# Kernel tuning notes

Measured on AMD Instinct MI355X. Metric: run time of the kernel, lower is better.

The kernel has to match this reference:

```python
import jax, jax.numpy as jnp
import numpy as np
from jax.scipy.special import xlogy

B, S, DIM, H = 2, 2048, 1024, 16
D = DIM // H          # head_dim = 64
B1 = B2 = 8           # monarch block sizes (hard-coded in source)
F = S // (B1 * B2)    # frames
NUM_ITERS = 2
EPS = 1e-6


def setup_inputs() -> dict:
    key = jax.random.key(0)
    ks = jax.random.split(key, 4)
    x = jax.random.normal(ks[0], (B, S, DIM), jnp.float32)
    # interleaved-pair RoPE tables, shape (S, D)
    pos = jnp.arange(S, dtype=jnp.float32)
    inv = 1.0 / (10000.0 ** (jnp.arange(0, D, 2, dtype=jnp.float32) / D))
    ang = pos[:, None] * inv[None, :]
    cos = jnp.repeat(jnp.cos(ang), 2, axis=-1)
    sin = jnp.repeat(jnp.sin(ang), 2, axis=-1)
    sc = 0.02
    wq = jax.random.normal(ks[1], (DIM, DIM), jnp.float32) * sc
    wk = jax.random.normal(ks[2], (DIM, DIM), jnp.float32) * sc
    wv = jax.random.normal(ks[3], (DIM, DIM), jnp.float32) * sc
    gq = jnp.ones((D,), jnp.float32)
    gk = jnp.ones((D,), jnp.float32)
    return {"x": x, "cos": cos, "sin": sin, "wq": wq, "wk": wk, "wv": wv,
            "gq": gq, "gk": gk}


def _rmsnorm(x, g, eps=EPS):
    return x * jax.lax.rsqrt(jnp.mean(x * x, axis=-1, keepdims=True) + eps) * g


def _rope(x, cos, sin):
    # x: (B,S,H,D); cos/sin: (S,D); rotate interleaved pairs
    xp = x.reshape(*x.shape[:-1], D // 2, 2)
    xr = jnp.stack([-xp[..., 1], xp[..., 0]], axis=-1).reshape(x.shape)
    return x * cos[None, :, None, :] + xr * sin[None, :, None, :]


def _monarch_forward(x, cos, sin, wq, wk, wv, gq, gk):
    b, s, dim = x.shape
    scale = D ** (-0.25)  # sm_scale_sqrt
    q = _rmsnorm((x @ wq.T).reshape(b, s, H, D), gq)
    k = _rmsnorm((x @ wk.T).reshape(b, s, H, D), gk)
    q = _rope(q, cos, sin) * scale
    k = _rope(k, cos, sin) * scale
    v = (x @ wv.T).reshape(b, s, H, D)

    # (b, frame, i=b1, j=b2, h, d)
    q = q.reshape(b, F, B1, B2, H, D)
    k = k.reshape(b, F, B1, B2, H, D)
    v = v.reshape(b, F, B1, B2, H, D)

    # causal frame mask: query frame g attends kv frames f <= g
    fmask = jnp.arange(F)[None, :] <= jnp.arange(F)[:, None]          # (G,F)
    mb = fmask[None, None, :, :, None, None, None]                    # (1,1,G,F,1,1,1)
    eye = jnp.eye(B1, dtype=x.dtype)                                   # (k,i)
    # L: (b,h,g,f,j,k,i), initialized to identity on allowed frames
    L = jnp.broadcast_to(jnp.where(mb, eye, 0.0), (b, H, F, F, B2, B1, B1))
    NEG = jnp.finfo(x.dtype).min

    R = None
    for _ in range(NUM_ITERS):
        aR = jnp.einsum('bhgfjki,bgijhd->bgfkjhd', L, q)
        bR = jnp.einsum('bgfkjhd,bfklhd->bhgfkjl', aR, k)
        cR = jnp.einsum('bhgfjki->bhgfkj', L)[..., None]
        R = jax.nn.softmax(bR / (cR + EPS), axis=-1)                  # (b,h,g,f,k,j,l)
        aL = jnp.einsum('bhgfkjl,bfklhd->bgfjkhd', R, k)
        bL = jnp.einsum('bgfjkhd,bgijhd->bhgfjki', aL, q)
        # cL[b,h,g,f,j,k] = sum_l xlogy(R)[b,h,g,f,k,j,l]
        cL = jnp.swapaxes(jnp.sum(xlogy(R, R), axis=-1), -1, -2)[..., None]
        M = jnp.where(mb, bL - cL, NEG)                               # (b,h,g,f,j,k,i)
        Mt = jnp.transpose(M, (0, 1, 2, 4, 6, 3, 5))                  # (b,h,g,j,i,f,k)
        Lf = jax.nn.softmax(Mt.reshape(b, H, F, B2, B1, F * B1), axis=-1)
        L = jnp.transpose(Lf.reshape(b, H, F, B2, B1, F, B1), (0, 1, 2, 5, 3, 6, 4))

    o = jnp.einsum('bhgfkjl,bfklhd->bgfjkhd', R, v)
    out = jnp.einsum('bhgfjki,bgfjkhd->bgijhd', L, o)                 # (b,G,i,j,h,d)
    return out.reshape(b, s, dim)


def reference(x, cos, sin, wq, wk, wv, gq, gk):
    return _monarch_forward(x, cos, sin, wq, wk, wv, gq, gk)
```

## Files before the change

### kernel.cpp

```cpp
#include <hip/hip_runtime.h>
#include <stdint.h>

typedef _Float16 f16;
typedef _Float16 half8 __attribute__((ext_vector_type(8)));
typedef _Float16 half4v __attribute__((ext_vector_type(4)));
typedef float f32x4 __attribute__((ext_vector_type(4)));

#define DEV static __device__ __forceinline__

DEV f32x4 mfma16(half8 a, half8 b, f32x4 c) {
  return __builtin_amdgcn_mfma_f32_16x16x32_f16(a, b, c, 0, 0, 0);
}

DEV void cp16(const f16* g, f16* l) {
  __builtin_amdgcn_global_load_lds(
      (const __attribute__((address_space(1))) void*)g,
      (__attribute__((address_space(3))) void*)l, 16, 0, 0);
}


__global__ __launch_bounds__(256) void k_cast(
    const float* __restrict__ x, const float* __restrict__ wq,
    const float* __restrict__ wk, const float* __restrict__ wv,
    f16* __restrict__ xh, f16* __restrict__ wcat) {
  const int64_t nx4 = 4194304 / 4;
  const int64_t nw4 = 1048576 / 4;
  int64_t stride = (int64_t)gridDim.x * blockDim.x;
  for (int64_t i = (int64_t)blockIdx.x * blockDim.x + threadIdx.x;
       i < nx4 + 3 * nw4; i += stride) {
    const float* src; f16* dst; int64_t off;
    if (i < nx4) { src = x; dst = xh; off = i; }
    else {
      int64_t r = i - nx4;
      int ws_ = (int)(r / nw4);
      off = r - (int64_t)ws_ * nw4;
      src = (ws_ == 0) ? wq : ((ws_ == 1) ? wk : wv);
      dst = wcat + (int64_t)ws_ * 1048576;
    }
    float4 v = ((const float4*)src)[off];
    half4v hh; hh[0] = (f16)v.x; hh[1] = (f16)v.y; hh[2] = (f16)v.z; hh[3] = (f16)v.w;
    ((half4v*)dst)[off] = hh;
  }
}

__global__ __launch_bounds__(256) void k_gemm(
    const f16* __restrict__ A, const f16* __restrict__ Bm,
    float* __restrict__ P) {
  __shared__ f16 As[128 * 64];
  __shared__ f16 Bs[128 * 64];
  const int t = threadIdx.x;
  const int wave = t >> 6, lane = t & 63, quad = lane >> 4, ln = lane & 15;
  const int tM = blockIdx.x / 24, tN = blockIdx.x % 24;
  const int wm = wave >> 1, wn = wave & 1;
  f32x4 acc[4][4];
#pragma unroll
  for (int a = 0; a < 4; ++a)
#pragma unroll
    for (int b = 0; b < 4; ++b) { f32x4 z = {0.f, 0.f, 0.f, 0.f}; acc[a][b] = z; }
  const int srow = t >> 3;
  const int c = (t & 7) ^ (srow & 7);
  const f16* Ag = A + (int64_t)(tM * 128 + srow) * 1024 + c * 8;
  const f16* Bg = Bm + (int64_t)(tN * 128 + srow) * 1024 + c * 8;
  for (int kt = 0; kt < 16; ++kt) {
    __syncthreads();
#pragma unroll
    for (int it = 0; it < 4; ++it) {
      cp16(Ag + (int64_t)it * 32 * 1024 + kt * 64, &As[it * 2048 + wave * 512]);
      cp16(Bg + (int64_t)it * 32 * 1024 + kt * 64, &Bs[it * 2048 + wave * 512]);
    }
    __syncthreads();
#pragma unroll
    for (int ks = 0; ks < 2; ++ks) {
      const int cs = ((ks * 4 + quad) ^ (ln & 7)) * 8;
      half8 bf[4];
#pragma unroll
      for (int tn = 0; tn < 4; ++tn)
        bf[tn] = *(const half8*)&Bs[(wn * 64 + tn * 16 + ln) * 64 + cs];
#pragma unroll
      for (int tm = 0; tm < 4; ++tm) {
        half8 af = *(const half8*)&As[(wm * 64 + tm * 16 + ln) * 64 + cs];
#pragma unroll
        for (int tn = 0; tn < 4; ++tn)
          acc[tm][tn] = mfma16(af, bf[tn], acc[tm][tn]);
      }
    }
  }
#pragma unroll
  for (int tm = 0; tm < 4; ++tm)
#pragma unroll
    for (int tn = 0; tn < 4; ++tn)
#pragma unroll
      for (int r2 = 0; r2 < 4; ++r2) {
        int row = tM * 128 + wm * 64 + tm * 16 + quad * 4 + r2;
        int col = tN * 128 + wn * 64 + tn * 16 + ln;
        P[(int64_t)row * 3072 + col] = acc[tm][tn][r2];
      }
}

__global__ __launch_bounds__(256) void k_epilogue(
    const float* __restrict__ P, const float* __restrict__ cosg,
    const float* __restrict__ sing, const float* __restrict__ gq,
    const float* __restrict__ gk, f16* __restrict__ qh,
    f16* __restrict__ kh, f16* __restrict__ vth) {
  __shared__ f16 vbuf[64 * 72];
  const int t = threadIdx.x;
  const int bid = blockIdx.x;
  const int st = bid & 31, h = (bid >> 5) & 15, b = bid >> 9;
  const int r = t >> 2, qt = t & 3, c0 = qt * 16;
  const int s = st * 64 + r;
  const int64_t rowbase = (int64_t)(b * 2048 + s) * 3072;
  const float scale = 0.35355339059327373f;
#pragma unroll
  for (int m = 0; m < 2; ++m) {
    const float* gv = (m == 0) ? gq : gk;
    const int colbase = m * 1024 + h * 64 + c0;
    float xv[16];
#pragma unroll
    for (int c = 0; c < 4; ++c) {
      float4 v4 = *(const float4*)&P[rowbase + colbase + c * 4];
      xv[c * 4 + 0] = v4.x; xv[c * 4 + 1] = v4.y;
      xv[c * 4 + 2] = v4.z; xv[c * 4 + 3] = v4.w;
    }
    float ss = 0.f;
#pragma unroll
    for (int c = 0; c < 16; ++c) ss += xv[c] * xv[c];
    ss += __shfl_xor(ss, 1, 64);
    ss += __shfl_xor(ss, 2, 64);
    float rs = rsqrtf(ss * (1.f / 64.f) + 1e-6f);
    alignas(16) f16 res[16];
#pragma unroll
    for (int ci = 0; ci < 16; ci += 2) {
      int d0 = c0 + ci, d1 = d0 + 1;
      float av = xv[ci] * rs * gv[d0];
      float bv = xv[ci + 1] * rs * gv[d1];
      float c0v = cosg[s * 64 + d0], c1v = cosg[s * 64 + d1];
      float s0v = sing[s * 64 + d0], s1v = sing[s * 64 + d1];
      res[ci]     = (f16)((av * c0v - bv * s0v) * scale);
      res[ci + 1] = (f16)((bv * c1v + av * s1v) * scale);
    }
    f16* dst = ((m == 0) ? qh : kh) + (int64_t)((b * 16 + h) * 2048 + s) * 64 + c0;
    *(half8*)dst = *(const half8*)&res[0];
    *(half8*)(dst + 8) = *(const half8*)&res[8];
  }
  {
    const int colbase = 2048 + h * 64 + c0;
#pragma unroll
    for (int c = 0; c < 4; ++c) {
      float4 v4 = *(const float4*)&P[rowbase + colbase + c * 4];
      vbuf[(c0 + c * 4 + 0) * 72 + r] = (f16)v4.x;
      vbuf[(c0 + c * 4 + 1) * 72 + r] = (f16)v4.y;
      vbuf[(c0 + c * 4 + 2) * 72 + r] = (f16)v4.z;
      vbuf[(c0 + c * 4 + 3) * 72 + r] = (f16)v4.w;
    }
    __syncthreads();
    const int d = t >> 2, sc = qt * 16;
    alignas(16) f16 tmp[16];
#pragma unroll
    for (int ci = 0; ci < 16; ++ci) tmp[ci] = vbuf[d * 72 + sc + ci];
    f16* dst = vth + (int64_t)(((b * 16 + h) * 32 + st) * 64 + d) * 64 + sc;
    *(half8*)dst = *(const half8*)&tmp[0];
    *(half8*)(dst + 8) = *(const half8*)&tmp[8];
  }
}

__global__ __launch_bounds__(64) void k_phase(
    const f16* __restrict__ qh, const f16* __restrict__ kh,
    float* __restrict__ Lg, f16* __restrict__ Rg,
    const f16* __restrict__ Pg, int iter) {
  __shared__ float Sw[4416];
  const int lane = threadIdx.x;
  const int quad = lane >> 4, ln = lane & 15;
  const int jr = lane >> 3, kr = lane & 7;

  const int bh = blockIdx.x / 528;
  const int rem = blockIdx.x - bh * 528;
  int g = (int)((sqrtf(8.f * (float)rem + 1.f) - 1.f) * 0.5f);
  while ((g + 1) * (g + 2) / 2 <= rem) ++g;
  while (g * (g + 1) / 2 > rem) --g;
  const int f = rem - g * (g + 1) / 2;

  const f16* qg = qh + (int64_t)(bh * 2048 + g * 64) * 64;
  const f16* kf = kh + (int64_t)(bh * 2048 + f * 64) * 64;
  const int64_t sbase = ((int64_t)bh * 528 + ((g * (g + 1)) >> 1) + f) * 512;
  float* Lp = Lg + sbase;

  half8 afr[2][4], bfr[2][4];
#pragma unroll
  for (int ks = 0; ks < 2; ++ks)
#pragma unroll
    for (int t4 = 0; t4 < 4; ++t4) {
      afr[ks][t4] = *(const half8*)&qg[(t4 * 16 + ln) * 64 + ks * 32 + quad * 8];
      bfr[ks][t4] = *(const half8*)&kf[(t4 * 16 + ln) * 64 + ks * 32 + quad * 8];
    }
  float p[8], cR = 0.f;
  if (iter) {
    half8 ph = *(const half8*)&Pg[sbase + lane * 8];
    p[0] = (float)ph[0]; p[2] = (float)ph[1]; p[4] = (float)ph[2]; p[6] = (float)ph[3];
    p[1] = (float)ph[4]; p[3] = (float)ph[5]; p[5] = (float)ph[6]; p[7] = (float)ph[7];
#pragma unroll
    for (int i = 0; i < 8; ++i) cR += p[i];
  }
  f32x4 acc[4][4];
#pragma unroll
  for (int a = 0; a < 4; ++a)
#pragma unroll
    for (int b = 0; b < 4; ++b) { f32x4 z = {0.f, 0.f, 0.f, 0.f}; acc[a][b] = z; }
#pragma unroll
  for (int ks = 0; ks < 2; ++ks)
#pragma unroll
    for (int mt = 0; mt < 4; ++mt)
#pragma unroll
      for (int nt = 0; nt < 4; ++nt)
        acc[mt][nt] = mfma16(afr[ks][mt], bfr[ks][nt], acc[mt][nt]);
  const int wbase = (quad >> 1) * 552 + (quad & 1) * 272 + (ln >> 3) * 8 + (ln & 7);
#pragma unroll
  for (int mt = 0; mt < 4; ++mt)
#pragma unroll
    for (int nt = 0; nt < 4; ++nt)
#pragma unroll
      for (int r2 = 0; r2 < 4; ++r2)
        Sw[wbase + mt * 1104 + nt * 16 + r2 * 68] = acc[mt][nt][r2];
  __syncthreads();
  float Sr[8][8];
  const int rb = jr * 68 + kr * 8;
#pragma unroll
  for (int i = 0; i < 8; ++i) {
    *(float4*)&Sr[i][0] = *(const float4*)&Sw[i * 552 + rb];
    *(float4*)&Sr[i][4] = *(const float4*)&Sw[i * 552 + rb + 4];
  }
  float va[8];
  if (!iter) {
    float4 d0 = *(const float4*)&Sw[kr * 552 + rb];
    float4 d1 = *(const float4*)&Sw[kr * 552 + rb + 4];
    va[0] = d0.x; va[1] = d0.y; va[2] = d0.z; va[3] = d0.w;
    va[4] = d1.x; va[5] = d1.y; va[6] = d1.z; va[7] = d1.w;
    const float sc = 1.f / (1.f + 1e-6f);
#pragma unroll
    for (int l = 0; l < 8; ++l) va[l] *= sc;
  } else {
    float bR[8];
#pragma unroll
    for (int l = 0; l < 8; ++l) bR[l] = 0.f;
#pragma unroll
    for (int i = 0; i < 8; ++i)
#pragma unroll
      for (int l = 0; l < 8; ++l) bR[l] += p[i] * Sr[i][l];
    const float rc = 1.f / (cR + 1e-6f);
#pragma unroll
    for (int l = 0; l < 8; ++l) va[l] = bR[l] * rc;
  }
  float mx = va[0];
#pragma unroll
  for (int l = 1; l < 8; ++l) mx = fmaxf(mx, va[l]);
  float ex[8], sm = 0.f;
#pragma unroll
  for (int l = 0; l < 8; ++l) { ex[l] = __expf(va[l] - mx); sm += ex[l]; }
  const float inv = 1.f / sm;
  float rr[8], rl = 0.f;
#pragma unroll
  for (int l = 0; l < 8; ++l) {
    rr[l] = ex[l] * inv;
    rl += rr[l] * __logf(fmaxf(rr[l], 1e-30f));
  }
  if (iter) {
    half8 r8;
#pragma unroll
    for (int l = 0; l < 8; ++l) r8[l] = (f16)rr[l];
    *(half8*)&Rg[sbase + kr * 64 + jr * 8] = r8;
  }
  float bl[8];
#pragma unroll
  for (int i = 0; i < 8; ++i) {
    float s = 0.f;
#pragma unroll
    for (int l = 0; l < 8; ++l) s += rr[l] * Sr[i][l];
    bl[i] = s - rl;
  }
  *(float4*)&Lp[lane * 8]     = *(const float4*)&bl[0];
  *(float4*)&Lp[lane * 8 + 4] = *(const float4*)&bl[4];
}

__global__ __launch_bounds__(256) void k_probs(
    const float* __restrict__ Lg, f16* __restrict__ Pg) {
  __shared__ float Ls[32 * 546];
  __shared__ float stt[128];
  const int t = threadIdx.x;
  const int g = 31 - (blockIdx.x & 31), bh = blockIdx.x >> 5;
  const int64_t sb = ((int64_t)bh * 528 + ((g * (g + 1)) >> 1)) * 512;
  const float* Lp = Lg + sb;
  for (int f = 0; f <= g; ++f) {
    const int o = 2 * t;
    *(float2*)&Ls[f * 546 + (o >> 6) * 68 + (o & 63)] = *(const float2*)&Lp[f * 512 + o];
  }
  __syncthreads();
  {
    const int p = t >> 2, sub = t & 3;
    const int base = (p >> 3) * 68 + (p & 7);
    float mx = -1e30f;
    for (int f = sub; f <= g; f += 4)
#pragma unroll
      for (int k_ = 0; k_ < 8; ++k_)
        mx = fmaxf(mx, Ls[f * 546 + base + k_ * 8]);
    mx = fmaxf(mx, __shfl_xor(mx, 1, 64));
    mx = fmaxf(mx, __shfl_xor(mx, 2, 64));
    float se = 0.f;
    for (int f = sub; f <= g; f += 4)
#pragma unroll
      for (int k_ = 0; k_ < 8; ++k_)
        se += __expf(Ls[f * 546 + base + k_ * 8] - mx);
    se += __shfl_xor(se, 1, 64);
    se += __shfl_xor(se, 2, 64);
    if (sub == 0) { stt[p * 2] = mx; stt[p * 2 + 1] = 1.f / se; }
  }
  __syncthreads();
  {
    const int r = t & 63, fq = t >> 6;
    const int j = r >> 3, k_ = r & 7;
    float mx[8], inv[8];
#pragma unroll
    for (int i = 0; i < 8; ++i) {
      mx[i] = stt[(j * 8 + i) * 2];
      inv[i] = stt[(j * 8 + i) * 2 + 1];
    }
    for (int fb = fq; fb <= g; fb += 4) {
      const float* row = &Ls[fb * 546 + j * 68 + k_ * 8];
      float pr[8];
#pragma unroll
      for (int i = 0; i < 8; ++i) pr[i] = __expf(row[i] - mx[i]) * inv[i];
      half8 st8;
      st8[0] = (f16)pr[0]; st8[1] = (f16)pr[2]; st8[2] = (f16)pr[4]; st8[3] = (f16)pr[6];
      st8[4] = (f16)pr[1]; st8[5] = (f16)pr[3]; st8[6] = (f16)pr[5]; st8[7] = (f16)pr[7];
      *(half8*)&Pg[sb + (int64_t)fb * 512 + r * 8] = st8;
    }
  }
}

__global__ __launch_bounds__(512) void k_out(
    const f16* __restrict__ Pg, const f16* __restrict__ Rg,
    const f16* __restrict__ vth, float* __restrict__ out) {
  __shared__ float red[64 * 64];
  const int t = threadIdx.x;
  const int wave = t >> 6, lane = t & 63, quad = lane >> 4, ln = lane & 15;
  const int fg = wave >> 2, dw = wave & 3;
  const int bh = blockIdx.x >> 4, G = blockIdx.x & 15;
  const int jl = ln & 7, ih = ln >> 3;
  const f16* vb = vth + ((int64_t)bh * 32 * 64 + dw * 16 + ln) * 64;

#pragma unroll 1
  for (int ph = 0; ph < 2; ++ph) {
    const int g = ph ? G : 31 - G;
    const int64_t sbase = ((int64_t)bh * 528 + ((g * (g + 1)) >> 1)) * 512;
    const f16* Pp = Pg + sbase;
    const f16* Rp = Rg + sbase;
    f32x4 oacc[4];
#pragma unroll
    for (int mt = 0; mt < 4; ++mt) { f32x4 z = {0.f, 0.f, 0.f, 0.f}; oacc[mt] = z; }

    half8 vA0, vA1, rA0, rA1; half4v pA0, pA1;
    half8 vB0, vB1, rB0, rB1; half4v pB0, pB1;
    auto loadit = [&](int f, half8& v0, half8& v1, half8& r0, half8& r1,
                      half4v& p0, half4v& p1) {
      const f16* Pf = Pp + f * 512;
      const f16* Rf = Rp + f * 512;
      const f16* vf = vb + (int64_t)f * 64 * 64;
      v0 = *(const half8*)&vf[quad * 8];
      v1 = *(const half8*)&vf[32 + quad * 8];
      r0 = *(const half8*)&Rf[quad * 64 + jl * 8];
      r1 = *(const half8*)&Rf[(4 + quad) * 64 + jl * 8];
      p0 = *(const half4v*)&Pf[jl * 64 + quad * 8 + ih * 4];
      p1 = *(const half4v*)&Pf[jl * 64 + (4 + quad) * 8 + ih * 4];
    };
    auto compit = [&](half8& v0, half8& v1, half8& r0, half8& r1,
                      half4v& p0, half4v& p1) {
#pragma unroll
      for (int mt = 0; mt < 4; ++mt) {
        const f16 Lh0 = p0[mt], Lh1 = p1[mt];
        half8 w0, w1;
#pragma unroll
        for (int l = 0; l < 8; ++l) { w0[l] = r0[l] * Lh0; w1[l] = r1[l] * Lh1; }
        oacc[mt] = mfma16(w0, v0, oacc[mt]);
        oacc[mt] = mfma16(w1, v1, oacc[mt]);
      }
    };
    int f = fg;
    if (f <= g) {
      loadit(f, vA0, vA1, rA0, rA1, pA0, pA1);
      while (true) {
        if (f + 2 <= g) {
          loadit(f + 2, vB0, vB1, rB0, rB1, pB0, pB1);
          compit(vA0, vA1, rA0, rA1, pA0, pA1);
          f += 2;
        } else { compit(vA0, vA1, rA0, rA1, pA0, pA1); break; }
        if (f + 2 <= g) {
          loadit(f + 2, vA0, vA1, rA0, rA1, pA0, pA1);
          compit(vB0, vB1, rB0, rB1, pB0, pB1);
          f += 2;
        } else { compit(vB0, vB1, rB0, rB1, pB0, pB1); break; }
      }
    }
    __syncthreads();
    if (fg == 1) {
#pragma unroll
      for (int mt = 0; mt < 4; ++mt)
#pragma unroll
        for (int r2 = 0; r2 < 4; ++r2)
          red[(dw * 16 + mt * 4 + r2) * 64 + lane] = oacc[mt][r2];
    }
    __syncthreads();
    if (fg == 0) {
#pragma unroll
      for (int mt = 0; mt < 4; ++mt)
#pragma unroll
        for (int r2 = 0; r2 < 4; ++r2)
          oacc[mt][r2] += red[(dw * 16 + mt * 4 + r2) * 64 + lane];
      float* ob = out + (int64_t)((bh >> 4) * 2048 + g * 64) * 1024 + (bh & 15) * 64;
#pragma unroll
      for (int mt = 0; mt < 4; ++mt)
#pragma unroll
        for (int r2 = 0; r2 < 4; ++r2)
          ob[(int64_t)(mt * 16 + quad * 4 + r2) * 1024 + dw * 16 + ln] = oacc[mt][r2];
    }
  }
}

extern "C" void kernel_launch(void* const* d_in, const int* in_sizes, int n_in,
                              void* d_out, int out_size, void* d_ws, size_t ws_size,
                              hipStream_t stream) {
  const float* x    = (const float*)d_in[0];
  const float* cosg = (const float*)d_in[1];
  const float* sing = (const float*)d_in[2];
  const float* wq   = (const float*)d_in[3];
  const float* wk   = (const float*)d_in[4];
  const float* wv   = (const float*)d_in[5];
  const float* gq   = (const float*)d_in[6];
  const float* gk   = (const float*)d_in[7];
  float* out = (float*)d_out;

  char* ws = (char*)d_ws;
  f16*   xh   = (f16*)(ws);
  f16*   wcat = (f16*)(ws + 8388608);
  float* P    = (float*)(ws + 14680064);
  f16*   Rg   = (f16*)(ws + 14680064);
  f16*   Pg   = (f16*)(ws + 31981568);
  f16*   qh   = (f16*)(ws + 65011712);
  f16*   kh   = (f16*)(ws + 73400320);
  f16*   vth  = (f16*)(ws + 81788928);
  float* Lg   = (float*)(ws + 90177536);

  hipLaunchKernelGGL(k_cast, dim3(1024), dim3(256), 0, stream, x, wq, wk, wv, xh, wcat);
  hipLaunchKernelGGL(k_gemm, dim3(768), dim3(256), 0, stream, xh, wcat, P);
  hipLaunchKernelGGL(k_epilogue, dim3(1024), dim3(256), 0, stream,
                     P, cosg, sing, gq, gk, qh, kh, vth);
  hipLaunchKernelGGL(k_phase, dim3(16896), dim3(64), 0, stream, qh, kh, Lg, Rg, Pg, 0);
  hipLaunchKernelGGL(k_probs, dim3(1024), dim3(256), 0, stream, Lg, Pg);
  hipLaunchKernelGGL(k_phase, dim3(16896), dim3(64), 0, stream, qh, kh, Lg, Rg, Pg, 1);
  hipLaunchKernelGGL(k_probs, dim3(1024), dim3(256), 0, stream, Lg, Pg);
  hipLaunchKernelGGL(k_out, dim3(512), dim3(512), 0, stream, Pg, Rg, vth, out);
}
```

Before: 291.6 us.

## Store phase logits and shared score tiles in fp16 instead of fp32

The L logits buffer written by k_phase and read by k_probs is stored as fp16 rather than fp32, halving that intermediate's global traffic. The shared-memory score tile in k_phase also becomes fp16 with a new padded layout, and rows are reread from LDS on demand instead of being held in a register array. This cuts LDS footprint and register pressure, but adds precision loss in the logits before the softmax over frames, and leaves values near large magnitudes more exposed to rounding.

```diff
diff --git a/kernel.cpp b/kernel.cpp
--- a/kernel.cpp
+++ b/kernel.cpp
@@ -165,9 +165,9 @@
 
 __global__ __launch_bounds__(64) void k_phase(
     const f16* __restrict__ qh, const f16* __restrict__ kh,
-    float* __restrict__ Lg, f16* __restrict__ Rg,
+    f16* __restrict__ Lg, f16* __restrict__ Rg,
     const f16* __restrict__ Pg, int iter) {
-  __shared__ float Sw[4416];
+  __shared__ f16 Sw[8 * 584];
   const int lane = threadIdx.x;
   const int quad = lane >> 4, ln = lane & 15;
   const int jr = lane >> 3, kr = lane & 7;
@@ -182,7 +182,7 @@
   const f16* qg = qh + (int64_t)(bh * 2048 + g * 64) * 64;
   const f16* kf = kh + (int64_t)(bh * 2048 + f * 64) * 64;
   const int64_t sbase = ((int64_t)bh * 528 + ((g * (g + 1)) >> 1) + f) * 512;
-  float* Lp = Lg + sbase;
+  f16* Lp = Lg + sbase;
 
   half8 afr[2][4], bfr[2][4];
 #pragma unroll
@@ -212,39 +212,36 @@
 #pragma unroll
       for (int nt = 0; nt < 4; ++nt)
         acc[mt][nt] = mfma16(afr[ks][mt], bfr[ks][nt], acc[mt][nt]);
-  const int wbase = (quad >> 1) * 552 + (quad & 1) * 272 + (ln >> 3) * 8 + (ln & 7);
-#pragma unroll
-  for (int mt = 0; mt < 4; ++mt)
-#pragma unroll
-    for (int nt = 0; nt < 4; ++nt)
-#pragma unroll
-      for (int r2 = 0; r2 < 4; ++r2)
-        Sw[wbase + mt * 1104 + nt * 16 + r2 * 68] = acc[mt][nt][r2];
+#pragma unroll
+  for (int nt = 0; nt < 4; ++nt) {
+    const int n = nt * 16 + ln;
+    const int cp = (n >> 3) * 8 + (n & 7);
+#pragma unroll
+    for (int mt = 0; mt < 4; ++mt)
+#pragma unroll
+      for (int r2 = 0; r2 < 4; ++r2) {
+        const int m = mt * 16 + quad * 4 + r2;
+        Sw[(m >> 3) * 584 + (m & 7) * 72 + cp] = (f16)acc[mt][nt][r2];
+      }
+  }
   __syncthreads();
-  float Sr[8][8];
-  const int rb = jr * 68 + kr * 8;
-#pragma unroll
-  for (int i = 0; i < 8; ++i) {
-    *(float4*)&Sr[i][0] = *(const float4*)&Sw[i * 552 + rb];
-    *(float4*)&Sr[i][4] = *(const float4*)&Sw[i * 552 + rb + 4];
-  }
+  const int rb = jr * 72 + kr * 8;
   float va[8];
   if (!iter) {
-    float4 d0 = *(const float4*)&Sw[kr * 552 + rb];
-    float4 d1 = *(const float4*)&Sw[kr * 552 + rb + 4];
-    va[0] = d0.x; va[1] = d0.y; va[2] = d0.z; va[3] = d0.w;
-    va[4] = d1.x; va[5] = d1.y; va[6] = d1.z; va[7] = d1.w;
+    half8 s8 = *(const half8*)&Sw[kr * 584 + rb];
     const float sc = 1.f / (1.f + 1e-6f);
 #pragma unroll
-    for (int l = 0; l < 8; ++l) va[l] *= sc;
+    for (int l = 0; l < 8; ++l) va[l] = (float)s8[l] * sc;
   } else {
     float bR[8];
 #pragma unroll
     for (int l = 0; l < 8; ++l) bR[l] = 0.f;
 #pragma unroll
-    for (int i = 0; i < 8; ++i)
-#pragma unroll
-      for (int l = 0; l < 8; ++l) bR[l] += p[i] * Sr[i][l];
+    for (int i = 0; i < 8; ++i) {
+      half8 s8 = *(const half8*)&Sw[i * 584 + rb];
+#pragma unroll
+      for (int l = 0; l < 8; ++l) bR[l] += p[i] * (float)s8[l];
+    }
     const float rc = 1.f / (cR + 1e-6f);
 #pragma unroll
     for (int l = 0; l < 8; ++l) va[l] = bR[l] * rc;
@@ -268,46 +265,47 @@
     for (int l = 0; l < 8; ++l) r8[l] = (f16)rr[l];
     *(half8*)&Rg[sbase + kr * 64 + jr * 8] = r8;
   }
-  float bl[8];
+  half8 blh;
 #pragma unroll
   for (int i = 0; i < 8; ++i) {
+    half8 s8 = *(const half8*)&Sw[i * 584 + rb];
     float s = 0.f;
 #pragma unroll
-    for (int l = 0; l < 8; ++l) s += rr[l] * Sr[i][l];
-    bl[i] = s - rl;
-  }
-  *(float4*)&Lp[lane * 8]     = *(const float4*)&bl[0];
-  *(float4*)&Lp[lane * 8 + 4] = *(const float4*)&bl[4];
+    for (int l = 0; l < 8; ++l) s += rr[l] * (float)s8[l];
+    blh[i] = (f16)(s - rl);
+  }
+  *(half8*)&Lp[lane * 8] = blh;
 }
 
 __global__ __launch_bounds__(256) void k_probs(
-    const float* __restrict__ Lg, f16* __restrict__ Pg) {
-  __shared__ float Ls[32 * 546];
+    const f16* __restrict__ Lg, f16* __restrict__ Pg) {
+  __shared__ f16 Ls[32 * 584];
   __shared__ float stt[128];
   const int t = threadIdx.x;
   const int g = 31 - (blockIdx.x & 31), bh = blockIdx.x >> 5;
   const int64_t sb = ((int64_t)bh * 528 + ((g * (g + 1)) >> 1)) * 512;
-  const float* Lp = Lg + sb;
+  const f16* Lp = Lg + sb;
   for (int f = 0; f <= g; ++f) {
     const int o = 2 * t;
-    *(float2*)&Ls[f * 546 + (o >> 6) * 68 + (o & 63)] = *(const float2*)&Lp[f * 512 + o];
+    *(uint32_t*)&Ls[f * 584 + (o >> 6) * 72 + (o & 63)] =
+        *(const uint32_t*)&Lp[f * 512 + o];
   }
   __syncthreads();
   {
     const int p = t >> 2, sub = t & 3;
-    const int base = (p >> 3) * 68 + (p & 7);
+    const int base = (p >> 3) * 72 + (p & 7);
     float mx = -1e30f;
     for (int f = sub; f <= g; f += 4)
 #pragma unroll
       for (int k_ = 0; k_ < 8; ++k_)
-        mx = fmaxf(mx, Ls[f * 546 + base + k_ * 8]);
+        mx = fmaxf(mx, (float)Ls[f * 584 + base + k_ * 8]);
     mx = fmaxf(mx, __shfl_xor(mx, 1, 64));
     mx = fmaxf(mx, __shfl_xor(mx, 2, 64));
     float se = 0.f;
     for (int f = sub; f <= g; f += 4)
 #pragma unroll
       for (int k_ = 0; k_ < 8; ++k_)
-        se += __expf(Ls[f * 546 + base + k_ * 8] - mx);
+        se += __expf((float)Ls[f * 584 + base + k_ * 8] - mx);
     se += __shfl_xor(se, 1, 64);
     se += __shfl_xor(se, 2, 64);
     if (sub == 0) { stt[p * 2] = mx; stt[p * 2 + 1] = 1.f / se; }
@@ -323,10 +321,10 @@
       inv[i] = stt[(j * 8 + i) * 2 + 1];
     }
     for (int fb = fq; fb <= g; fb += 4) {
-      const float* row = &Ls[fb * 546 + j * 68 + k_ * 8];
+      half8 row8 = *(const half8*)&Ls[fb * 584 + j * 72 + k_ * 8];
       float pr[8];
 #pragma unroll
-      for (int i = 0; i < 8; ++i) pr[i] = __expf(row[i] - mx[i]) * inv[i];
+      for (int i = 0; i < 8; ++i) pr[i] = __expf((float)row8[i] - mx[i]) * inv[i];
       half8 st8;
       st8[0] = (f16)pr[0]; st8[1] = (f16)pr[2]; st8[2] = (f16)pr[4]; st8[3] = (f16)pr[6];
       st8[4] = (f16)pr[1]; st8[5] = (f16)pr[3]; st8[6] = (f16)pr[5]; st8[7] = (f16)pr[7];
@@ -445,7 +443,7 @@
   f16*   qh   = (f16*)(ws + 65011712);
   f16*   kh   = (f16*)(ws + 73400320);
   f16*   vth  = (f16*)(ws + 81788928);
-  float* Lg   = (float*)(ws + 90177536);
+  f16*   Lg   = (f16*)(ws + 90177536);
 
   hipLaunchKernelGGL(k_cast, dim3(1024), dim3(256), 0, stream, x, wq, wk, wv, xh, wcat);
   hipLaunchKernelGGL(k_gemm, dim3(768), dim3(256), 0, stream, xh, wcat, P);
```

New measurement: 265.3 us. 9.0% less time.
